# Kernel optimization log

Hardware: AMD Instinct MI355X
Metric: run time of the kernel (lower is better)

Reference implementation:

```python
import jax, jax.numpy as jnp
import numpy as np

N_TEMPS = 800
TEMP_STEP = 0.00125
TARGET_VAL = 0.2666666667
TOL = 0.01


def setup_inputs() -> dict:
    key = jax.random.key(0)
    logits = jax.random.normal(key, (128, 1000), dtype=jnp.float32)
    return {"logits": logits}


def reference(logits) -> jnp.ndarray:
    B, C = logits.shape
    dt = logits.dtype
    # ECE-style 3-bin boundaries: linspace(0, 1, 4)
    bin_lowers = jnp.array([0.0, 1.0 / 3.0, 2.0 / 3.0], dtype=dt)
    bin_uppers = jnp.array([1.0 / 3.0, 2.0 / 3.0, 1.0], dtype=dt)
    new_bin_lowers = jnp.array([0.8, 0.86666666666, 0.93333333333], dtype=dt)

    # original confidence = max softmax prob per sample
    conf = jnp.max(jax.nn.softmax(logits, axis=1), axis=1)  # [B]

    # bin assignment: uppers > conf and lowers <= conf
    in_bin = (bin_uppers[None, :] > conf[:, None]) & (bin_lowers[None, :] <= conf[:, None])
    bin_idx = jnp.argmax(in_bin, axis=1)  # [B]

    # target confidence after compression
    new_conf = new_bin_lowers[bin_idx] + (1.0 / 15.0) * ((conf - bin_lowers[bin_idx]) / TARGET_VAL)  # [B]

    # temperature grid 1.0, 0.99875, ... (800 values)
    temps = 1.0 - TEMP_STEP * jnp.arange(N_TEMPS, dtype=dt)  # [T]

    # vectorized sweep: scaled logits [B, T, C]
    scaled = logits[:, None, :] / temps[None, :, None]
    # max softmax prob = exp(max_logit - logsumexp)
    conf_t = jnp.exp(jnp.max(scaled, axis=-1) - jax.nn.logsumexp(scaled, axis=-1))  # [B, T]

    ok = jnp.abs(conf_t - new_conf[:, None]) <= TOL  # [B, T]
    found = jnp.any(ok, axis=1)                      # [B]
    j_first = jnp.argmax(ok, axis=1)                 # first matching temperature index
    chosen_temp = temps[j_first]                     # [B]

    out = jnp.where(found[:, None], logits / chosen_temp[:, None], logits)
    return out
```

## Files before the change

### kernel.cpp

```cpp
#include <hip/hip_runtime.h>
#include <math.h>

#define NB 128
#define NC 1000
#define NT 800

__device__ __forceinline__ float block_reduce_sum(float v, float* sred, float* sbcast) {
    for (int o = 32; o > 0; o >>= 1) v += __shfl_xor(v, o, 64);
    int tid = threadIdx.x;
    if ((tid & 63) == 0) sred[tid >> 6] = v;
    __syncthreads();
    if (tid == 0) *sbcast = (sred[0] + sred[1]) + (sred[2] + sred[3]);
    __syncthreads();
    return *sbcast;
}

__device__ __forceinline__ float eval_S(const float* __restrict__ srow, float t, float m,
                                        float* sred, float* sbcast) {
    float m2 = m / t;
    float s = 0.f;
    for (int i = threadIdx.x; i < NC; i += 256)
        s += expf(srow[i] / t - m2);
    return block_reduce_sum(s, sred, sbcast);
}

__device__ __forceinline__ float conft_from_S(float S, float t, float m) {
    float m2 = t == 1.0f ? m : (m / t);
    float lse = m2 + logf(S);
    return expf(m2 - lse);
}

__global__ __launch_bounds__(256) void logitcomp_kernel(const float* __restrict__ logits,
                                                        float* __restrict__ out) {
    __shared__ float srow[NC];
    __shared__ float sred[4];
    __shared__ float sbcast;

    int r = blockIdx.x;
    int tid = threadIdx.x;
    const float* row = logits + r * NC;

    for (int i = tid; i < NC; i += 256) srow[i] = row[i];
    __syncthreads();

    float mv = -INFINITY;
    for (int i = tid; i < NC; i += 256) mv = fmaxf(mv, srow[i]);
    for (int o = 32; o > 0; o >>= 1) mv = fmaxf(mv, __shfl_xor(mv, o, 64));
    if ((tid & 63) == 0) sred[tid >> 6] = mv;
    __syncthreads();
    if (tid == 0) sbcast = fmaxf(fmaxf(sred[0], sred[1]), fmaxf(sred[2], sred[3]));
    __syncthreads();
    float m = sbcast;

    float S1 = eval_S(srow, 1.0f, m, sred, &sbcast);
    float conf = 1.0f / S1;

    const float third = (float)(1.0 / 3.0);
    const float twoth = (float)(2.0 / 3.0);
    bool b0 = (third > conf) && (0.0f <= conf);
    bool b1 = (twoth > conf) && (third <= conf);
    bool b2 = (1.0f > conf) && (twoth <= conf);
    int idx = b0 ? 0 : (b1 ? 1 : (b2 ? 2 : 0));
    float bl = (idx == 0) ? 0.0f : ((idx == 1) ? third : twoth);
    float nb = (idx == 0) ? 0.8f : ((idx == 1) ? (float)0.86666666666 : (float)0.93333333333);
    const float TARGET = (float)0.2666666667;
    const float K = (float)(1.0 / 15.0);
    float nc = nb + K * ((conf - bl) / TARGET);

    int lo = 0, count = NT;
    while (count > 0) {
        int step = count >> 1;
        int mid = lo + step;
        float t = 1.0f - 0.00125f * (float)mid;
        float S = eval_S(srow, t, m, sred, &sbcast);
        float conft = conft_from_S(S, t, m);
        bool ok = fabsf(conft - nc) <= 0.01f;
        bool below = (conft < nc) && !ok;
        if (below) { lo = mid + 1; count -= step + 1; }
        else        count = step;
    }

    bool found = false;
    float tch = 1.0f;
    if (lo < NT) {
        float t = 1.0f - 0.00125f * (float)lo;
        float S = eval_S(srow, t, m, sred, &sbcast);
        float conft = conft_from_S(S, t, m);
        found = fabsf(conft - nc) <= 0.01f;
        tch = t;
    }

    float* orow = out + r * NC;
    for (int i = tid; i < NC; i += 256) {
        float l = srow[i];
        orow[i] = found ? (l / tch) : l;
    }
}

extern "C" void kernel_launch(void* const* d_in, const int* in_sizes, int n_in,
                              void* d_out, int out_size, void* d_ws, size_t ws_size,
                              hipStream_t stream) {
    const float* logits = (const float*)d_in[0];
    float* out = (float*)d_out;
    logitcomp_kernel<<<NB, 256, 0, stream>>>(logits, out);
}
```

Measured before the change: 65.14 us.

## Replace binary temperature search with 17-way parallel search across waves

The block grows to 1024 threads (16 waves). Each round of the temperature search now evaluates 16 candidate temperatures at once, one per wave, and splits the interval 17 ways instead of 2. This cuts the number of sequential search rounds and block-wide barriers from about ten to roughly three. In exchange each wave does a serial reduction over 1000 logits, and only 128 blocks run, so occupancy per CU stays low.

Result: slower. 66.89 us (+2.7%).

```diff
diff --git a/kernel.cpp b/kernel.cpp
--- a/kernel.cpp
+++ b/kernel.cpp
@@ -4,56 +4,49 @@
 #define NB 128
 #define NC 1000
 #define NT 800
+#define NWAVES 16
+#define BLK 1024
 
-__device__ __forceinline__ float block_reduce_sum(float v, float* sred, float* sbcast) {
-    for (int o = 32; o > 0; o >>= 1) v += __shfl_xor(v, o, 64);
-    int tid = threadIdx.x;
-    if ((tid & 63) == 0) sred[tid >> 6] = v;
-    __syncthreads();
-    if (tid == 0) *sbcast = (sred[0] + sred[1]) + (sred[2] + sred[3]);
-    __syncthreads();
-    return *sbcast;
-}
-
-__device__ __forceinline__ float eval_S(const float* __restrict__ srow, float t, float m,
-                                        float* sred, float* sbcast) {
-    float m2 = m / t;
-    float s = 0.f;
-    for (int i = threadIdx.x; i < NC; i += 256)
-        s += expf(srow[i] / t - m2);
-    return block_reduce_sum(s, sred, sbcast);
-}
-
-__device__ __forceinline__ float conft_from_S(float S, float t, float m) {
-    float m2 = t == 1.0f ? m : (m / t);
-    float lse = m2 + logf(S);
-    return expf(m2 - lse);
-}
-
-__global__ __launch_bounds__(256) void logitcomp_kernel(const float* __restrict__ logits,
+__global__ __launch_bounds__(BLK) void logitcomp_kernel(const float* __restrict__ logits,
                                                         float* __restrict__ out) {
     __shared__ float srow[NC];
-    __shared__ float sred[4];
+    __shared__ float sred[NWAVES];
+    __shared__ float sconf[NWAVES];
     __shared__ float sbcast;
 
     int r = blockIdx.x;
     int tid = threadIdx.x;
+    int wave = tid >> 6;
+    int lane = tid & 63;
     const float* row = logits + r * NC;
 
-    for (int i = tid; i < NC; i += 256) srow[i] = row[i];
+    for (int i = tid; i < NC; i += BLK) srow[i] = row[i];
     __syncthreads();
 
-    float mv = -INFINITY;
-    for (int i = tid; i < NC; i += 256) mv = fmaxf(mv, srow[i]);
+    float mv = (tid < NC) ? srow[tid] : -INFINITY;
     for (int o = 32; o > 0; o >>= 1) mv = fmaxf(mv, __shfl_xor(mv, o, 64));
-    if ((tid & 63) == 0) sred[tid >> 6] = mv;
+    if (lane == 0) sred[wave] = mv;
     __syncthreads();
-    if (tid == 0) sbcast = fmaxf(fmaxf(sred[0], sred[1]), fmaxf(sred[2], sred[3]));
+    if (tid == 0) {
+        float mm = sred[0];
+        for (int w = 1; w < NWAVES; ++w) mm = fmaxf(mm, sred[w]);
+        sbcast = mm;
+    }
     __syncthreads();
     float m = sbcast;
+    __syncthreads();
 
-    float S1 = eval_S(srow, 1.0f, m, sred, &sbcast);
-    float conf = 1.0f / S1;
+    float s1 = (tid < NC) ? expf(srow[tid] - m) : 0.f;
+    for (int o = 32; o > 0; o >>= 1) s1 += __shfl_xor(s1, o, 64);
+    if (lane == 0) sred[wave] = s1;
+    __syncthreads();
+    if (tid == 0) {
+        float S = 0.f;
+        for (int w = 0; w < NWAVES; ++w) S += sred[w];
+        sbcast = S;
+    }
+    __syncthreads();
+    float conf = 1.0f / sbcast;
 
     const float third = (float)(1.0 / 3.0);
     const float twoth = (float)(2.0 / 3.0);
@@ -67,31 +60,60 @@
     const float K = (float)(1.0 / 15.0);
     float nc = nb + K * ((conf - bl) / TARGET);
 
-    int lo = 0, count = NT;
-    while (count > 0) {
-        int step = count >> 1;
-        int mid = lo + step;
-        float t = 1.0f - 0.00125f * (float)mid;
-        float S = eval_S(srow, t, m, sred, &sbcast);
-        float conft = conft_from_S(S, t, m);
-        bool ok = fabsf(conft - nc) <= 0.01f;
-        bool below = (conft < nc) && !ok;
-        if (below) { lo = mid + 1; count -= step + 1; }
-        else        count = step;
+    int lo = 0, hi = NT;
+    bool okhi = false;
+
+    while (lo < hi) {
+        int count = hi - lo;
+        int np = (count <= NWAVES) ? count : NWAVES;
+
+        if (wave < np) {
+            int p = (count <= NWAVES) ? (lo + wave)
+                                      : (lo + ((wave + 1) * count) / 17);
+            float t = 1.0f - 0.00125f * (float)p;
+            float m2 = m / t;
+            float sw = 0.f;
+            for (int i = lane; i < NC; i += 64)
+                sw += expf(srow[i] / t - m2);
+            for (int o = 32; o > 0; o >>= 1) sw += __shfl_xor(sw, o, 64);
+            if (lane == 0) {
+                float lse = m2 + logf(sw);
+                sconf[wave] = expf(m2 - lse);
+            }
+        }
+        __syncthreads();
+
+        int firsti = -1;
+        float cfound = 0.f;
+        for (int i = 0; i < np; ++i) {
+            float c = sconf[i];
+            bool oki = fabsf(c - nc) <= 0.01f;
+            bool below = (c < nc) && !oki;
+            if (!below) { firsti = i; cfound = c; break; }
+        }
+        __syncthreads();
+
+        if (count <= NWAVES) {
+            if (firsti >= 0) { hi = lo + firsti; okhi = fabsf(cfound - nc) <= 0.01f; }
+            lo = hi;
+        } else {
+            if (firsti < 0) {
+                lo = lo + (NWAVES * count) / 17 + 1;
+            } else {
+                int pf = lo + ((firsti + 1) * count) / 17;
+                int nl = (firsti > 0) ? (lo + (firsti * count) / 17 + 1) : lo;
+                hi = pf;
+                okhi = fabsf(cfound - nc) <= 0.01f;
+                lo = nl;
+            }
+        }
     }
 
-    bool found = false;
-    float tch = 1.0f;
-    if (lo < NT) {
-        float t = 1.0f - 0.00125f * (float)lo;
-        float S = eval_S(srow, t, m, sred, &sbcast);
-        float conft = conft_from_S(S, t, m);
-        found = fabsf(conft - nc) <= 0.01f;
-        tch = t;
-    }
+    bool found = okhi && (hi < NT);
+    float tch = 1.0f - 0.00125f * (float)hi;
 
     float* orow = out + r * NC;
-    for (int i = tid; i < NC; i += 256) {
+    for (int i = tid; i < NC; i += BLK) {
         float l = srow[i];
         orow[i] = found ? (l / tch) : l;
     }
@@ -102,5 +124,5 @@
                               hipStream_t stream) {
     const float* logits = (const float*)d_in[0];
     float* out = (float*)d_out;
-    logitcomp_kernel<<<NB, 256, 0, stream>>>(logits, out);
+    logitcomp_kernel<<<NB, BLK, 0, stream>>>(logits, out);
 }
```
